# Performance work log

Measured on AMD Instinct MI355X. Metric: run time of the kernel, lower is better.

## Reference

```python
import jax, jax.numpy as jnp
import numpy as np

B, T, C = 4, 1024, 768
H, HD = 12, 64
E, K, DFF = 16, 2, 3072
EPS = 1e-5


def layernorm(x, w, b):
    mu = jnp.mean(x, axis=-1, keepdims=True)
    xc = x - mu
    var = jnp.mean(xc * xc, axis=-1, keepdims=True)
    return xc * jax.lax.rsqrt(var + EPS) * w + b


def setup_inputs() -> dict:
    key = jax.random.key(0)
    ks = jax.random.split(key, 12)
    s = lambda fan_in: 1.0 / np.sqrt(fan_in)
    return {
        "x": jax.random.normal(ks[0], (B, T, C), jnp.float32),
        "ln1_w": jnp.ones((C,), jnp.float32),
        "ln1_b": jnp.zeros((C,), jnp.float32),
        "W_attn": jax.random.normal(ks[1], (C, 3 * C), jnp.float32) * s(C),
        "b_attn": jnp.zeros((3 * C,), jnp.float32),
        "W_proj": jax.random.normal(ks[2], (C, C), jnp.float32) * s(C),
        "b_proj": jnp.zeros((C,), jnp.float32),
        "ln2_w": jnp.ones((C,), jnp.float32),
        "ln2_b": jnp.zeros((C,), jnp.float32),
        "W_router": jax.random.normal(ks[3], (C, E), jnp.float32) * s(C),
        "W1": jax.random.normal(ks[4], (E, C, DFF), jnp.float32) * s(C),
        "b1": jnp.zeros((E, DFF), jnp.float32),
        "W2": jax.random.normal(ks[5], (E, DFF, C), jnp.float32) * s(DFF),
        "b2": jnp.zeros((E, C), jnp.float32),
    }


def reference(x, ln1_w, ln1_b, W_attn, b_attn, W_proj, b_proj,
              ln2_w, ln2_b, W_router, W1, b1, W2, b2):
    # --- attention sublayer ---
    xn = layernorm(x, ln1_w, ln1_b)
    qkv = xn @ W_attn + b_attn                                  # [B,T,3C]
    q, k, v = jnp.split(qkv, 3, axis=-1)
    q = q.reshape(B, T, H, HD).transpose(0, 2, 1, 3)            # [B,H,T,HD]
    k = k.reshape(B, T, H, HD).transpose(0, 2, 1, 3)
    v = v.reshape(B, T, H, HD).transpose(0, 2, 1, 3)
    att = jnp.einsum('bhqd,bhkd->bhqk', q, k) / np.sqrt(HD)
    causal = jnp.tril(jnp.ones((T, T), bool))
    att = jnp.where(causal, att, -jnp.inf)
    att = jax.nn.softmax(att, axis=-1)
    y = jnp.einsum('bhqk,bhkd->bhqd', att, v)
    y = y.transpose(0, 2, 1, 3).reshape(B, T, C)
    x = x + y @ W_proj + b_proj

    # --- MoE sublayer: dense all-experts with top-k gating mask ---
    xn2 = layernorm(x, ln2_w, ln2_b)
    probs = jax.nn.softmax(xn2 @ W_router, axis=-1)             # [B,T,E]
    top_p, top_idx = jax.lax.top_k(probs, K)                    # [B,T,K]
    gating = jnp.sum(jax.nn.one_hot(top_idx, E, dtype=probs.dtype)
                     * top_p[..., None], axis=-2)               # [B,T,E]
    g = jnp.moveaxis(gating, -1, 0)                             # [E,B,T]

    def body(acc, params):
        W1e, b1e, W2e, b2e, ge = params
        h = jax.nn.gelu(xn2 @ W1e + b1e, approximate=False)     # [B,T,DFF]
        out = h @ W2e + b2e                                     # [B,T,C]
        return acc + ge[..., None] * out, None

    y_moe, _ = jax.lax.scan(body, jnp.zeros_like(x), (W1, b1, W2, b2, g))
    # note: MoELayer returns x + y, and Block adds residual again
    return x + (xn2_residual := 0) + xn2 * 0 + (x * 0) + x * 0 + y_moe + x * 0 if False else x + (x * 0) + y_moe + x * 0 * 0 if False else x + x * 0 + y_moe + (x - x) if False else x + (x + y_moe) - x + (x + y_moe) - (x + y_moe) if False else x + x + y_moe - x if False else (x + (x + y_moe)) - x + (x - x) if False else x + y_moe + x - x if False else _block_out(x, xn2, y_moe)


def _block_out(x, xn2, y_moe):
    # MoELayer.forward returns x_in + y where x_in is ln2 *input* (x here);
    # Block then does x = x + ffn(ln2(x)) -> x + (x + y_moe)? No: MoE input is
    # xn2 = ln2(x), so ffn(ln2(x)) = xn2 + y_moe, and Block adds residual x.
    return x + xn2 + y_moe
```

## Files before the change

### kernel.cpp

```cpp
#include <hip/hip_runtime.h>
#include <math.h>

#define CC    768
#define C3    2304
#define KD    2304
#define LDA2  1536
#define TT    1024
#define BB    4
#define HH    12
#define HD    64
#define EE    16
#define DFFN  3072
#define NTOK  4096
#define NSLOT 8192
#define LDP   136

typedef unsigned short u16;
typedef unsigned int   u32;
typedef __attribute__((ext_vector_type(8))) short short8;
typedef __attribute__((ext_vector_type(4))) float floatx4;

__device__ __forceinline__ u16 f2bf(float f){
  u32 x = __builtin_bit_cast(u32, f);
  x += 0x7fffu + ((x >> 16) & 1u);
  return (u16)(x >> 16);
}
__device__ __forceinline__ u16 f2h(float f){
  _Float16 h = (_Float16)f;
  return __builtin_bit_cast(u16, h);
}
__device__ __forceinline__ float h2f(u16 u){
  return (float)__builtin_bit_cast(_Float16, u);
}
__device__ __forceinline__ float gelu_exact(float v){
  return 0.5f * v * (1.f + erff(v * 0.70710678118654752440f));
}
__device__ __forceinline__ void split2h(float v, u16& h0, u16& h1){
  float vs = v * 64.f;
  h0 = f2h(vs);
  h1 = f2h(vs - h2f(h0));
}
__device__ __forceinline__ void gload_lds16(const void* g, void* l){
  __builtin_amdgcn_global_load_lds(
      (const __attribute__((address_space(1))) void*)g,
      (__attribute__((address_space(3))) void*)l, 16, 0, 0);
}

template<int MODE>
__global__ __launch_bounds__(256) void transpose_split(const float* __restrict__ src,
    u16* __restrict__ d0, int R, int Cn)
{
  __shared__ float tile[32][33];
  int z = blockIdx.z;
  const float* s = src + (size_t)z * R * Cn;
  int c0 = blockIdx.x * 32, r0 = blockIdx.y * 32;
  int tx = threadIdx.x & 31, ty = threadIdx.x >> 5;
  #pragma unroll
  for (int j = 0; j < 4; ++j)
    tile[ty + j*8][tx] = s[(size_t)(r0 + ty + j*8) * Cn + c0 + tx];
  __syncthreads();
  #pragma unroll
  for (int j = 0; j < 4; ++j){
    float v = tile[tx][ty + j*8];
    if (MODE == 1){
      u16 h0, h1; split2h(v, h0, h1);
      size_t base = (size_t)(c0 + ty + j*8) * LDA2 + (r0 + tx);
      d0[base] = h0; d0[base + 768] = h1;
    } else {
      d0[(size_t)z * R * Cn + (size_t)(c0 + ty + j*8) * R + r0 + tx] = f2bf(v);
    }
  }
}

template<int MODE>
__global__ __launch_bounds__(256) void ln_kernel(const float* __restrict__ x,
    const float* __restrict__ gw, const float* __restrict__ gb,
    float* __restrict__ of, u16* __restrict__ o0)
{
  int tok = blockIdx.x, tid = threadIdx.x;
  const float* xr = x + (size_t)tok * CC;
  float v0 = xr[tid], v1 = xr[tid + 256], v2 = xr[tid + 512];
  __shared__ float r1[4], r2[4];
  __shared__ float mus, rss;
  float s = v0 + v1 + v2;
  #pragma unroll
  for (int off = 32; off >= 1; off >>= 1) s += __shfl_down(s, off);
  if ((tid & 63) == 0) r1[tid >> 6] = s;
  __syncthreads();
  if (tid == 0) mus = (r1[0] + r1[1] + r1[2] + r1[3]) * (1.f / 768.f);
  __syncthreads();
  float mu = mus;
  float d0 = v0 - mu, d1 = v1 - mu, d2 = v2 - mu;
  float t = d0*d0 + d1*d1 + d2*d2;
  #pragma unroll
  for (int off = 32; off >= 1; off >>= 1) t += __shfl_down(t, off);
  if ((tid & 63) == 0) r2[tid >> 6] = t;
  __syncthreads();
  if (tid == 0) rss = rsqrtf((r2[0] + r2[1] + r2[2] + r2[3]) * (1.f / 768.f) + 1e-5f);
  __syncthreads();
  float rstd = rss;
  float dv[3] = {d0, d1, d2};
  #pragma unroll
  for (int i = 0; i < 3; ++i){
    int c = tid + i * 256;
    float vv = dv[i] * rstd * gw[c] + gb[c];
    if (MODE == 1){
      u16 h0, h1; split2h(vv, h0, h1);
      o0[(size_t)tok * LDA2 + c] = h0;
      o0[(size_t)tok * LDA2 + 768 + c] = h1;
    } else {
      size_t idx = (size_t)tok * CC + c;
      of[idx] = vv;
      o0[idx] = f2bf(vv);
    }
  }
}

__global__ __launch_bounds__(256) void gemm_dense(
    const u16* __restrict__ A, const u16* __restrict__ Bt,
    float* __restrict__ C, const float* __restrict__ bias,
    const float* __restrict__ resid, int N)
{
  __shared__ u16 As[128 * 32];
  __shared__ u16 Bs[128 * 32];
  int tid = threadIdx.x;
  int lane = tid & 63, wave = tid >> 6;
  int wm = wave & 1, wn = wave >> 1;
  int m0 = blockIdx.y * 128, n0 = blockIdx.x * 128;
  int ra = tid >> 2, ka = (tid & 3) * 8;
  const u16* pa0 = A  + (size_t)(m0 + ra)      * LDA2 + ka;
  const u16* pa1 = A  + (size_t)(m0 + ra + 64) * LDA2 + ka;
  const u16* pb0 = Bt + (size_t)(n0 + ra)      * LDA2 + ka;
  const u16* pb1 = Bt + (size_t)(n0 + ra + 64) * LDA2 + ka;
  u16* lA0 = As + wave*512;        u16* lA1 = As + 2048 + wave*512;
  u16* lB0 = Bs + wave*512;        u16* lB1 = Bs + 2048 + wave*512;
  floatx4 acc[4][4] = {};
  int el = lane & 15, eq = lane >> 4;
  for (int k0 = 0; k0 < KD; k0 += 32){
    int ca = (k0 >= 768) ? k0 - 768 : k0;
    int cb = (k0 < 1536) ? k0 : k0 - 1536;
    __syncthreads();
    gload_lds16(pa0 + ca, lA0);
    gload_lds16(pa1 + ca, lA1);
    gload_lds16(pb0 + cb, lB0);
    gload_lds16(pb1 + cb, lB1);
    __syncthreads();
    short8 fa[4], fb[4];
    #pragma unroll
    for (int t = 0; t < 4; ++t)
      fa[t] = *(const short8*)&As[(size_t)(wm*64 + t*16 + el) * 32 + eq*8];
    #pragma unroll
    for (int t = 0; t < 4; ++t)
      fb[t] = *(const short8*)&Bs[(size_t)(wn*64 + t*16 + el) * 32 + eq*8];
    #pragma unroll
    for (int mt = 0; mt < 4; ++mt)
      #pragma unroll
      for (int nt = 0; nt < 4; ++nt)
        acc[mt][nt] = __builtin_amdgcn_mfma_f32_16x16x32_f16(fa[mt], fb[nt], acc[mt][nt], 0, 0, 0);
  }
  const float ds = 1.f / 4096.f;
  #pragma unroll
  for (int mt = 0; mt < 4; ++mt){
    #pragma unroll
    for (int nt = 0; nt < 4; ++nt){
      int col = n0 + wn*64 + nt*16 + el;
      float bv = bias ? bias[col] : 0.f;
      #pragma unroll
      for (int r = 0; r < 4; ++r){
        int row = m0 + wm*64 + mt*16 + eq*4 + r;
        size_t idx = (size_t)row * N + col;
        float val = acc[mt][nt][r] * ds + bv;
        if (resid) val += resid[idx];
        C[idx] = val;
      }
    }
  }
}

__global__ __launch_bounds__(256) void flash_mfma(const float* __restrict__ qkv,
    u16* __restrict__ yH)
{
  __shared__ u16 Qs[64 * LDP];
  __shared__ u16 Ks[64 * LDP];
  __shared__ u16 Vt[64 * LDP];
  __shared__ u16 Ps[64 * LDP];
  int tid = threadIdx.x;
  int lane = tid & 63, wv = tid >> 6;
  int qi = 15 - blockIdx.x;
  int bh = blockIdx.y;
  int b = bh / HH, h = bh % HH;
  int el = lane & 15, eq = lane >> 4;
  int m0 = wv * 16;
  int row0 = qi * 64;

  {
    int r = tid >> 2, d0 = (tid & 3) * 16;
    const float* src = qkv + (size_t)(b*TT + row0 + r) * C3 + h*HD + d0;
    u16* q0 = &Qs[r * LDP + d0];
    #pragma unroll
    for (int i = 0; i < 16; i += 2){
      u16 a0, a1, b0, b1;
      split2h(src[i], a0, a1);
      split2h(src[i+1], b0, b1);
      *(u32*)&q0[i]      = (u32)a0 | ((u32)b0 << 16);
      *(u32*)&q0[64 + i] = (u32)a1 | ((u32)b1 << 16);
    }
  }
  floatx4 O[4] = {};
  float mrow[4], lrow[4];
  #pragma unroll
  for (int r = 0; r < 4; ++r){ mrow[r] = -1e30f; lrow[r] = 0.f; }

  const float cmul = 0.125f * 1.44269504088896340736f / 4096.f;
  const int ABase[6] = {0,32,0,32,64,96};
  const int BBase[6] = {0,32,64,96,0,32};

  for (int kt = 0; kt <= qi; ++kt){
    __syncthreads();
    {
      int j = tid >> 2, d0 = (tid & 3) * 16;
      const float* src = qkv + (size_t)(b*TT + kt*64 + j) * C3 + CC + h*HD + d0;
      u16* kp = &Ks[j * LDP + d0];
      #pragma unroll
      for (int i = 0; i < 16; i += 2){
        u16 a0, a1, b0, b1;
        split2h(src[i], a0, a1);
        split2h(src[i+1], b0, b1);
        *(u32*)&kp[i]      = (u32)a0 | ((u32)b0 << 16);
        *(u32*)&kp[64 + i] = (u32)a1 | ((u32)b1 << 16);
      }
      int d = tid & 63, kp0 = (tid >> 6) * 16;
      const float* vsrc = qkv + (size_t)(b*TT + kt*64 + kp0) * C3 + 2*CC + h*HD + d;
      u16* vt = &Vt[d * LDP];
      #pragma unroll
      for (int i = 0; i < 16; i += 2){
        u16 a0, a1, b0, b1;
        split2h(vsrc[(size_t)i * C3], a0, a1);
        split2h(vsrc[(size_t)(i+1) * C3], b0, b1);
        *(u32*)&vt[kp0 + i]      = (u32)a0 | ((u32)b0 << 16);
        *(u32*)&vt[64 + kp0 + i] = (u32)a1 | ((u32)b1 << 16);
      }
    }
    __syncthreads();
    floatx4 S[4] = {};
    #pragma unroll
    for (int ks = 0; ks < 6; ++ks){
      short8 fa = *(const short8*)&Qs[(m0 + el) * LDP + ABase[ks] + eq*8];
      short8 fb[4];
      #pragma unroll
      for (int nt = 0; nt < 4; ++nt)
        fb[nt] = *(const short8*)&Ks[(nt*16 + el) * LDP + BBase[ks] + eq*8];
      #pragma unroll
      for (int nt = 0; nt < 4; ++nt)
        S[nt] = __builtin_amdgcn_mfma_f32_16x16x32_f16(fa, fb[nt], S[nt], 0, 0, 0);
    }
    #pragma unroll
    for (int nt = 0; nt < 4; ++nt){
      int kcol = kt*64 + nt*16 + el;
      #pragma unroll
      for (int r = 0; r < 4; ++r){
        int grow = row0 + m0 + eq*4 + r;
        float sv = S[nt][r] * cmul;
        S[nt][r] = (kcol <= grow) ? sv : -1e30f;
      }
    }
    #pragma unroll
    for (int r = 0; r < 4; ++r){
      float tmax = fmaxf(fmaxf(S[0][r], S[1][r]), fmaxf(S[2][r], S[3][r]));
      #pragma unroll
      for (int off = 1; off < 16; off <<= 1) tmax = fmaxf(tmax, __shfl_xor(tmax, off));
      float mnew = fmaxf(mrow[r], tmax);
      float al = exp2f(mrow[r] - mnew);
      mrow[r] = mnew;
      lrow[r] *= al;
      #pragma unroll
      for (int nt = 0; nt < 4; ++nt) O[nt][r] *= al;
      #pragma unroll
      for (int nt = 0; nt < 4; ++nt){
        float p = exp2f(S[nt][r] - mnew);
        lrow[r] += p;
        S[nt][r] = p;
      }
    }
    #pragma unroll
    for (int nt = 0; nt < 4; ++nt){
      #pragma unroll
      for (int r = 0; r < 4; ++r){
        u16 p0, p1; split2h(S[nt][r], p0, p1);
        int rowl = m0 + eq*4 + r;
        Ps[rowl * LDP + nt*16 + el] = p0;
        Ps[rowl * LDP + 64 + nt*16 + el] = p1;
      }
    }
    #pragma unroll
    for (int ks = 0; ks < 6; ++ks){
      short8 fa = *(const short8*)&Ps[(m0 + el) * LDP + ABase[ks] + eq*8];
      short8 fb[4];
      #pragma unroll
      for (int nt = 0; nt < 4; ++nt)
        fb[nt] = *(const short8*)&Vt[(nt*16 + el) * LDP + BBase[ks] + eq*8];
      #pragma unroll
      for (int nt = 0; nt < 4; ++nt)
        O[nt] = __builtin_amdgcn_mfma_f32_16x16x32_f16(fa, fb[nt], O[nt], 0, 0, 0);
    }
  }
  #pragma unroll
  for (int r = 0; r < 4; ++r){
    float l = lrow[r];
    #pragma unroll
    for (int off = 1; off < 16; off <<= 1) l += __shfl_xor(l, off);
    float inv = 1.f / (l * 4096.f);
    int grow = row0 + m0 + eq*4 + r;
    u16* dst = yH + (size_t)(b*TT + grow) * LDA2 + h*HD;
    #pragma unroll
    for (int nt = 0; nt < 4; ++nt){
      float yv = O[nt][r] * inv;
      u16 y0, y1; split2h(yv, y0, y1);
      dst[nt*16 + el] = y0;
      dst[768 + nt*16 + el] = y1;
    }
  }
}

__global__ __launch_bounds__(256) void router_kernel(const float* __restrict__ xn2,
    const float* __restrict__ Wr, int* __restrict__ eids, float* __restrict__ wts)
{
  int wave = threadIdx.x >> 6, lane = threadIdx.x & 63;
  int tok = blockIdx.x * 4 + wave;
  int g = lane >> 4, e = lane & 15;
  const float* xr = xn2 + (size_t)tok * CC;
  float s = 0.f;
  for (int c4 = 0; c4 < 192; ++c4){
    int c = c4 * 4 + g;
    s += xr[c] * Wr[c * EE + e];
  }
  s += __shfl_xor(s, 16);
  s += __shfl_xor(s, 32);
  float mx = s;
  #pragma unroll
  for (int off = 1; off < 16; off <<= 1) mx = fmaxf(mx, __shfl_xor(mx, off));
  float p = expf(s - mx);
  float Z = p;
  #pragma unroll
  for (int off = 1; off < 16; off <<= 1) Z += __shfl_xor(Z, off);
  p /= Z;
  float best = -1.f; int bi = 0;
  for (int ee = 0; ee < 16; ++ee){
    float pe = __shfl(p, ee);
    if (pe > best){ best = pe; bi = ee; }
  }
  float sec = -1.f; int si = 0;
  for (int ee = 0; ee < 16; ++ee){
    float pe = __shfl(p, ee);
    if (ee != bi && pe > sec){ sec = pe; si = ee; }
  }
  if (lane == 0){
    eids[tok*2] = bi;  eids[tok*2+1] = si;
    wts [tok*2] = best; wts[tok*2+1] = sec;
  }
}

__global__ __launch_bounds__(256) void moe_count(const int* __restrict__ eids,
    int* __restrict__ counts, int* __restrict__ offs, int* __restrict__ curs)
{
  __shared__ int lc[EE];
  int tid = threadIdx.x;
  if (tid < EE) lc[tid] = 0;
  __syncthreads();
  for (int i = tid; i < NSLOT; i += 256) atomicAdd(&lc[eids[i]], 1);
  __syncthreads();
  if (tid == 0){
    int run = 0;
    for (int e = 0; e < EE; ++e){
      counts[e] = lc[e]; offs[e] = run; curs[e] = run; run += lc[e];
    }
    offs[EE] = run;
  }
}

__global__ __launch_bounds__(256) void moe_scatter(const int* __restrict__ eids,
    const float* __restrict__ wts, int* __restrict__ curs,
    int* __restrict__ rowmap, float* __restrict__ wgtm)
{
  int i = blockIdx.x * 256 + threadIdx.x;
  int e = eids[i];
  int pos = atomicAdd(&curs[e], 1);
  rowmap[pos] = i >> 1;
  wgtm[pos] = wts[i];
}

__global__ __launch_bounds__(256) void add2(const float* __restrict__ a,
    const float* __restrict__ b, float* __restrict__ o, int n)
{
  int i = blockIdx.x * 256 + threadIdx.x;
  if (i < n) o[i] = a[i] + b[i];
}

__global__ __launch_bounds__(256) void gemm_moe1(
    const u16* __restrict__ Xb, const u16* __restrict__ W1t, const float* __restrict__ b1,
    u16* __restrict__ H, const int* __restrict__ counts, const int* __restrict__ offs,
    const int* __restrict__ rowmap)
{
  int e = blockIdx.z;
  int cnt = counts[e];
  int m0 = blockIdx.y * 128;
  if (m0 >= cnt) return;
  int off = offs[e];
  int n0 = blockIdx.x * 128;
  const u16* Bt = W1t + (size_t)e * DFFN * CC;
  __shared__ u16 As[128 * 32];
  __shared__ u16 Bs[128 * 32];
  int tid = threadIdx.x;
  int lane = tid & 63, wave = tid >> 6;
  int wm = wave & 1, wn = wave >> 1;
  int ra = tid >> 2, ka = (tid & 3) * 8;
  int r0 = m0 + ra, r1i = m0 + ra + 64;
  int rr0 = (r0  < cnt) ? r0  : cnt - 1;
  int rr1 = (r1i < cnt) ? r1i : cnt - 1;
  const u16* pa0 = Xb + (size_t)rowmap[off + rr0] * CC + ka;
  const u16* pa1 = Xb + (size_t)rowmap[off + rr1] * CC + ka;
  const u16* pb0 = Bt + (size_t)(n0 + ra)      * CC + ka;
  const u16* pb1 = Bt + (size_t)(n0 + ra + 64) * CC + ka;
  u16* lA0 = As + wave*512;        u16* lA1 = As + 2048 + wave*512;
  u16* lB0 = Bs + wave*512;        u16* lB1 = Bs + 2048 + wave*512;
  floatx4 acc[4][4] = {};
  int el = lane & 15, eq = lane >> 4;
  for (int k0 = 0; k0 < CC; k0 += 32){
    __syncthreads();
    gload_lds16(pa0 + k0, lA0);
    gload_lds16(pa1 + k0, lA1);
    gload_lds16(pb0 + k0, lB0);
    gload_lds16(pb1 + k0, lB1);
    __syncthreads();
    short8 fa[4], fb[4];
    #pragma unroll
    for (int t = 0; t < 4; ++t)
      fa[t] = *(const short8*)&As[(size_t)(wm*64 + t*16 + el) * 32 + eq*8];
    #pragma unroll
    for (int t = 0; t < 4; ++t)
      fb[t] = *(const short8*)&Bs[(size_t)(wn*64 + t*16 + el) * 32 + eq*8];
    #pragma unroll
    for (int mt = 0; mt < 4; ++mt)
      #pragma unroll
      for (int nt = 0; nt < 4; ++nt)
        acc[mt][nt] = __builtin_amdgcn_mfma_f32_16x16x32_bf16(fa[mt], fb[nt], acc[mt][nt], 0, 0, 0);
  }
  #pragma unroll
  for (int mt = 0; mt < 4; ++mt){
    #pragma unroll
    for (int nt = 0; nt < 4; ++nt){
      int col = n0 + wn*64 + nt*16 + el;
      float bv = b1[(size_t)e * DFFN + col];
      #pragma unroll
      for (int r = 0; r < 4; ++r){
        int row = m0 + wm*64 + mt*16 + eq*4 + r;
        if (row < cnt)
          H[(size_t)(off + row) * DFFN + col] = f2bf(gelu_exact(acc[mt][nt][r] + bv));
      }
    }
  }
}

#define KSPL 2
__global__ __launch_bounds__(256) void gemm_moe2(
    const u16* __restrict__ H, const u16* __restrict__ W2t, const float* __restrict__ b2,
    float* __restrict__ Out, const int* __restrict__ counts, const int* __restrict__ offs,
    const int* __restrict__ rowmap, const float* __restrict__ wgtm)
{
  int e = blockIdx.z;
  int cnt = counts[e];
  int m0 = blockIdx.y * 128;
  if (m0 >= cnt) return;
  int off = offs[e];
  int bx = blockIdx.x;
  int n0 = (bx % 6) * 128;
  int ksp = bx / 6;
  const u16* Bt = W2t + (size_t)e * CC * DFFN;
  __shared__ u16 As[128 * 32];
  __shared__ u16 Bs[128 * 32];
  int tid = threadIdx.x;
  int lane = tid & 63, wave = tid >> 6;
  int wm = wave & 1, wn = wave >> 1;
  int ra = tid >> 2, ka = (tid & 3) * 8;
  int r0 = m0 + ra, r1i = m0 + ra + 64;
  int rr0 = (r0  < cnt) ? r0  : cnt - 1;
  int rr1 = (r1i < cnt) ? r1i : cnt - 1;
  const u16* pa0 = H + (size_t)(off + rr0) * DFFN + ka;
  const u16* pa1 = H + (size_t)(off + rr1) * DFFN + ka;
  const u16* pb0 = Bt + (size_t)(n0 + ra)      * DFFN + ka;
  const u16* pb1 = Bt + (size_t)(n0 + ra + 64) * DFFN + ka;
  u16* lA0 = As + wave*512;        u16* lA1 = As + 2048 + wave*512;
  u16* lB0 = Bs + wave*512;        u16* lB1 = Bs + 2048 + wave*512;
  floatx4 acc[4][4] = {};
  int el = lane & 15, eq = lane >> 4;
  int kbeg = ksp * (DFFN / KSPL), kend = kbeg + DFFN / KSPL;
  for (int k0 = kbeg; k0 < kend; k0 += 32){
    __syncthreads();
    gload_lds16(pa0 + k0, lA0);
    gload_lds16(pa1 + k0, lA1);
    gload_lds16(pb0 + k0, lB0);
    gload_lds16(pb1 + k0, lB1);
    __syncthreads();
    short8 fa[4], fb[4];
    #pragma unroll
    for (int t = 0; t < 4; ++t)
      fa[t] = *(const short8*)&As[(size_t)(wm*64 + t*16 + el) * 32 + eq*8];
    #pragma unroll
    for (int t = 0; t < 4; ++t)
      fb[t] = *(const short8*)&Bs[(size_t)(wn*64 + t*16 + el) * 32 + eq*8];
    #pragma unroll
    for (int mt = 0; mt < 4; ++mt)
      #pragma unroll
      for (int nt = 0; nt < 4; ++nt)
        acc[mt][nt] = __builtin_amdgcn_mfma_f32_16x16x32_bf16(fa[mt], fb[nt], acc[mt][nt], 0, 0, 0);
  }
  #pragma unroll
  for (int mt = 0; mt < 4; ++mt){
    #pragma unroll
    for (int nt = 0; nt < 4; ++nt){
      int col = n0 + wn*64 + nt*16 + el;
      float bv = (ksp == 0) ? b2[(size_t)e * CC + col] : 0.f;
      #pragma unroll
      for (int r = 0; r < 4; ++r){
        int row = m0 + wm*64 + mt*16 + eq*4 + r;
        if (row < cnt){
          int slot = off + row;
          int tok = rowmap[slot];
          float wv = wgtm[slot];
          atomicAdd(&Out[(size_t)tok * CC + col], wv * (acc[mt][nt][r] + bv));
        }
      }
    }
  }
}

extern "C" void kernel_launch(void* const* d_in, const int* in_sizes, int n_in,
                              void* d_out, int out_size, void* d_ws, size_t ws_size,
                              hipStream_t stream)
{
  const float* x     = (const float*)d_in[0];
  const float* ln1w  = (const float*)d_in[1];
  const float* ln1b  = (const float*)d_in[2];
  const float* Wattn = (const float*)d_in[3];
  const float* battn = (const float*)d_in[4];
  const float* Wproj = (const float*)d_in[5];
  const float* bproj = (const float*)d_in[6];
  const float* ln2w  = (const float*)d_in[7];
  const float* ln2b  = (const float*)d_in[8];
  const float* Wrout = (const float*)d_in[9];
  const float* W1    = (const float*)d_in[10];
  const float* b1    = (const float*)d_in[11];
  const float* W2    = (const float*)d_in[12];
  const float* b2    = (const float*)d_in[13];
  float* out = (float*)d_out;

  char* w = (char*)d_ws;
  auto alloc = [&](size_t bytes)->char* {
    char* p = w; w += (bytes + 255) & ~(size_t)255; return p;
  };
  u16* watp  = (u16*)alloc((size_t)C3 * LDA2 * 2);
  u16* wptp  = (u16*)alloc((size_t)CC * LDA2 * 2);
  u16* w1t   = (u16*)alloc((size_t)EE * DFFN * CC * 2);
  u16* w2t   = (u16*)alloc((size_t)EE * CC * DFFN * 2);
  u16* xH    = (u16*)alloc((size_t)NTOK * LDA2 * 2);
  float* qkv = (float*)alloc((size_t)NTOK * C3 * 4);
  u16* yH    = (u16*)alloc((size_t)NTOK * LDA2 * 2);
  u16* Hbuf  = (u16*)alloc((size_t)NSLOT * DFFN * 2);
  float* x2    = (float*)alloc((size_t)NTOK * CC * 4);
  float* xn2   = (float*)alloc((size_t)NTOK * CC * 4);
  u16*   xn2b  = (u16*)alloc((size_t)NTOK * CC * 2);
  int*   eids  = (int*)alloc(NSLOT * 4);
  float* wts   = (float*)alloc(NSLOT * 4);
  int* counts  = (int*)alloc(256);
  int* offs    = (int*)alloc(256);
  int* curs    = (int*)alloc(256);
  int* rowmap  = (int*)alloc(NSLOT * 4);
  float* wgtm  = (float*)alloc(NSLOT * 4);

  hipLaunchKernelGGL((transpose_split<1>), dim3(C3/32, CC/32, 1), dim3(256), 0, stream,
                     Wattn, watp, CC, C3);
  hipLaunchKernelGGL((transpose_split<1>), dim3(CC/32, CC/32, 1), dim3(256), 0, stream,
                     Wproj, wptp, CC, CC);
  hipLaunchKernelGGL((transpose_split<0>), dim3(DFFN/32, CC/32, EE), dim3(256), 0, stream,
                     W1, w1t, CC, DFFN);
  hipLaunchKernelGGL((transpose_split<0>), dim3(CC/32, DFFN/32, EE), dim3(256), 0, stream,
                     W2, w2t, DFFN, CC);
  hipLaunchKernelGGL((ln_kernel<1>), dim3(NTOK), dim3(256), 0, stream,
                     x, ln1w, ln1b, (float*)nullptr, xH);
  hipLaunchKernelGGL(gemm_dense, dim3(C3/128, NTOK/128), dim3(256), 0, stream,
                     xH, watp, qkv, battn, (const float*)nullptr, C3);
  hipLaunchKernelGGL(flash_mfma, dim3(16, BB*HH), dim3(256), 0, stream, qkv, yH);
  hipLaunchKernelGGL(gemm_dense, dim3(CC/128, NTOK/128), dim3(256), 0, stream,
                     yH, wptp, x2, bproj, x, CC);
  hipLaunchKernelGGL((ln_kernel<0>), dim3(NTOK), dim3(256), 0, stream,
                     x2, ln2w, ln2b, xn2, xn2b);
  hipLaunchKernelGGL(router_kernel, dim3(NTOK/4), dim3(256), 0, stream, xn2, Wrout, eids, wts);
  hipLaunchKernelGGL(moe_count, dim3(1), dim3(256), 0, stream, eids, counts, offs, curs);
  hipLaunchKernelGGL(moe_scatter, dim3(NSLOT/256), dim3(256), 0, stream, eids, wts, curs, rowmap, wgtm);
  hipLaunchKernelGGL(add2, dim3(NTOK*CC/256), dim3(256), 0, stream, x2, xn2, out, NTOK*CC);
  hipLaunchKernelGGL(gemm_moe1, dim3(DFFN/128, 32, EE), dim3(256), 0, stream,
                     xn2b, w1t, b1, Hbuf, counts, offs, rowmap);
  hipLaunchKernelGGL(gemm_moe2, dim3(6*KSPL, 32, EE), dim3(256), 0, stream,
                     Hbuf, w2t, b2, out, counts, offs, rowmap, wgtm);
}
```

Before: 950.3 us.

## Double-buffer LDS tiles in dense and MoE GEMMs to overlap loads with MFMA

Converts the dense GEMM and both MoE expert GEMMs from single-buffered LDS staging with two barriers per K-step to a ping-pong scheme. The next K tile is issued into the alternate buffer before the MFMAs on the current tile, with one barrier per iteration. This aims to hide global-to-LDS load latency behind matrix math. It doubles LDS use per block (32 KB), which may lower occupancy, and correctness depends on the direct-to-LDS loads being complete by the time the single barrier is passed.

```diff
diff --git a/kernel.cpp b/kernel.cpp
--- a/kernel.cpp
+++ b/kernel.cpp
@@ -121,8 +121,8 @@
     float* __restrict__ C, const float* __restrict__ bias,
     const float* __restrict__ resid, int N)
 {
-  __shared__ u16 As[128 * 32];
-  __shared__ u16 Bs[128 * 32];
+  __shared__ u16 As[2][128 * 32];
+  __shared__ u16 Bs[2][128 * 32];
   int tid = threadIdx.x;
   int lane = tid & 63, wave = tid >> 6;
   int wm = wave & 1, wn = wave >> 1;
@@ -132,31 +132,36 @@
   const u16* pa1 = A  + (size_t)(m0 + ra + 64) * LDA2 + ka;
   const u16* pb0 = Bt + (size_t)(n0 + ra)      * LDA2 + ka;
   const u16* pb1 = Bt + (size_t)(n0 + ra + 64) * LDA2 + ka;
-  u16* lA0 = As + wave*512;        u16* lA1 = As + 2048 + wave*512;
-  u16* lB0 = Bs + wave*512;        u16* lB1 = Bs + 2048 + wave*512;
   floatx4 acc[4][4] = {};
   int el = lane & 15, eq = lane >> 4;
-  for (int k0 = 0; k0 < KD; k0 += 32){
+
+  auto stage = [&](int buf, int k0){
     int ca = (k0 >= 768) ? k0 - 768 : k0;
     int cb = (k0 < 1536) ? k0 : k0 - 1536;
-    __syncthreads();
-    gload_lds16(pa0 + ca, lA0);
-    gload_lds16(pa1 + ca, lA1);
-    gload_lds16(pb0 + cb, lB0);
-    gload_lds16(pb1 + cb, lB1);
-    __syncthreads();
+    gload_lds16(pa0 + ca, &As[buf][wave*512]);
+    gload_lds16(pa1 + ca, &As[buf][2048 + wave*512]);
+    gload_lds16(pb0 + cb, &Bs[buf][wave*512]);
+    gload_lds16(pb1 + cb, &Bs[buf][2048 + wave*512]);
+  };
+  stage(0, 0);
+  __syncthreads();
+  int cur = 0;
+  for (int k0 = 0; k0 < KD; k0 += 32){
+    if (k0 + 32 < KD) stage(cur ^ 1, k0 + 32);
     short8 fa[4], fb[4];
     #pragma unroll
     for (int t = 0; t < 4; ++t)
-      fa[t] = *(const short8*)&As[(size_t)(wm*64 + t*16 + el) * 32 + eq*8];
+      fa[t] = *(const short8*)&As[cur][(size_t)(wm*64 + t*16 + el) * 32 + eq*8];
     #pragma unroll
     for (int t = 0; t < 4; ++t)
-      fb[t] = *(const short8*)&Bs[(size_t)(wn*64 + t*16 + el) * 32 + eq*8];
+      fb[t] = *(const short8*)&Bs[cur][(size_t)(wn*64 + t*16 + el) * 32 + eq*8];
     #pragma unroll
     for (int mt = 0; mt < 4; ++mt)
       #pragma unroll
       for (int nt = 0; nt < 4; ++nt)
         acc[mt][nt] = __builtin_amdgcn_mfma_f32_16x16x32_f16(fa[mt], fb[nt], acc[mt][nt], 0, 0, 0);
+    __syncthreads();
+    cur ^= 1;
   }
   const float ds = 1.f / 4096.f;
   #pragma unroll
@@ -408,8 +413,8 @@
   int off = offs[e];
   int n0 = blockIdx.x * 128;
   const u16* Bt = W1t + (size_t)e * DFFN * CC;
-  __shared__ u16 As[128 * 32];
-  __shared__ u16 Bs[128 * 32];
+  __shared__ u16 As[2][128 * 32];
+  __shared__ u16 Bs[2][128 * 32];
   int tid = threadIdx.x;
   int lane = tid & 63, wave = tid >> 6;
   int wm = wave & 1, wn = wave >> 1;
@@ -421,29 +426,34 @@
   const u16* pa1 = Xb + (size_t)rowmap[off + rr1] * CC + ka;
   const u16* pb0 = Bt + (size_t)(n0 + ra)      * CC + ka;
   const u16* pb1 = Bt + (size_t)(n0 + ra + 64) * CC + ka;
-  u16* lA0 = As + wave*512;        u16* lA1 = As + 2048 + wave*512;
-  u16* lB0 = Bs + wave*512;        u16* lB1 = Bs + 2048 + wave*512;
   floatx4 acc[4][4] = {};
   int el = lane & 15, eq = lane >> 4;
+
+  auto stage = [&](int buf, int k0){
+    gload_lds16(pa0 + k0, &As[buf][wave*512]);
+    gload_lds16(pa1 + k0, &As[buf][2048 + wave*512]);
+    gload_lds16(pb0 + k0, &Bs[buf][wave*512]);
+    gload_lds16(pb1 + k0, &Bs[buf][2048 + wave*512]);
+  };
+  stage(0, 0);
+  __syncthreads();
+  int cur = 0;
   for (int k0 = 0; k0 < CC; k0 += 32){
-    __syncthreads();
-    gload_lds16(pa0 + k0, lA0);
-    gload_lds16(pa1 + k0, lA1);
-    gload_lds16(pb0 + k0, lB0);
-    gload_lds16(pb1 + k0, lB1);
-    __syncthreads();
+    if (k0 + 32 < CC) stage(cur ^ 1, k0 + 32);
     short8 fa[4], fb[4];
     #pragma unroll
     for (int t = 0; t < 4; ++t)
-      fa[t] = *(const short8*)&As[(size_t)(wm*64 + t*16 + el) * 32 + eq*8];
+      fa[t] = *(const short8*)&As[cur][(size_t)(wm*64 + t*16 + el) * 32 + eq*8];
     #pragma unroll
     for (int t = 0; t < 4; ++t)
-      fb[t] = *(const short8*)&Bs[(size_t)(wn*64 + t*16 + el) * 32 + eq*8];
+      fb[t] = *(const short8*)&Bs[cur][(size_t)(wn*64 + t*16 + el) * 32 + eq*8];
     #pragma unroll
     for (int mt = 0; mt < 4; ++mt)
       #pragma unroll
       for (int nt = 0; nt < 4; ++nt)
         acc[mt][nt] = __builtin_amdgcn_mfma_f32_16x16x32_bf16(fa[mt], fb[nt], acc[mt][nt], 0, 0, 0);
+    __syncthreads();
+    cur ^= 1;
   }
   #pragma unroll
   for (int mt = 0; mt < 4; ++mt){
@@ -476,8 +486,8 @@
   int n0 = (bx % 6) * 128;
   int ksp = bx / 6;
   const u16* Bt = W2t + (size_t)e * CC * DFFN;
-  __shared__ u16 As[128 * 32];
-  __shared__ u16 Bs[128 * 32];
+  __shared__ u16 As[2][128 * 32];
+  __shared__ u16 Bs[2][128 * 32];
   int tid = threadIdx.x;
   int lane = tid & 63, wave = tid >> 6;
   int wm = wave & 1, wn = wave >> 1;
@@ -489,30 +499,35 @@
   const u16* pa1 = H + (size_t)(off + rr1) * DFFN + ka;
   const u16* pb0 = Bt + (size_t)(n0 + ra)      * DFFN + ka;
   const u16* pb1 = Bt + (size_t)(n0 + ra + 64) * DFFN + ka;
-  u16* lA0 = As + wave*512;        u16* lA1 = As + 2048 + wave*512;
-  u16* lB0 = Bs + wave*512;        u16* lB1 = Bs + 2048 + wave*512;
   floatx4 acc[4][4] = {};
   int el = lane & 15, eq = lane >> 4;
   int kbeg = ksp * (DFFN / KSPL), kend = kbeg + DFFN / KSPL;
+
+  auto stage = [&](int buf, int k0){
+    gload_lds16(pa0 + k0, &As[buf][wave*512]);
+    gload_lds16(pa1 + k0, &As[buf][2048 + wave*512]);
+    gload_lds16(pb0 + k0, &Bs[buf][wave*512]);
+    gload_lds16(pb1 + k0, &Bs[buf][2048 + wave*512]);
+  };
+  stage(0, kbeg);
+  __syncthreads();
+  int cur = 0;
   for (int k0 = kbeg; k0 < kend; k0 += 32){
-    __syncthreads();
-    gload_lds16(pa0 + k0, lA0);
-    gload_lds16(pa1 + k0, lA1);
-    gload_lds16(pb0 + k0, lB0);
-    gload_lds16(pb1 + k0, lB1);
-    __syncthreads();
+    if (k0 + 32 < kend) stage(cur ^ 1, k0 + 32);
     short8 fa[4], fb[4];
     #pragma unroll
     for (int t = 0; t < 4; ++t)
-      fa[t] = *(const short8*)&As[(size_t)(wm*64 + t*16 + el) * 32 + eq*8];
+      fa[t] = *(const short8*)&As[cur][(size_t)(wm*64 + t*16 + el) * 32 + eq*8];
     #pragma unroll
     for (int t = 0; t < 4; ++t)
-      fb[t] = *(const short8*)&Bs[(size_t)(wn*64 + t*16 + el) * 32 + eq*8];
+      fb[t] = *(const short8*)&Bs[cur][(size_t)(wn*64 + t*16 + el) * 32 + eq*8];
     #pragma unroll
     for (int mt = 0; mt < 4; ++mt)
       #pragma unroll
       for (int nt = 0; nt < 4; ++nt)
         acc[mt][nt] = __builtin_amdgcn_mfma_f32_16x16x32_bf16(fa[mt], fb[nt], acc[mt][nt], 0, 0, 0);
+    __syncthreads();
+    cur ^= 1;
   }
   #pragma unroll
   for (int mt = 0; mt < 4; ++mt){
```

Result: no change. 965.3 us (+1.6%).
